# Optimization experiments

Measured on AMD Instinct MI355X. Metric: run time of the kernel, lower is better.

## Reference

```python
import jax, jax.numpy as jnp
import numpy as np

N = 50000   # nodes
E = 800000  # edges (avg degree 16)
DIMS = [(128, 128), (128, 128), (128, 64)]  # (in, out) per SAGEConv layer
EPS_BN = 1e-5
EPS_NORM = 1e-12


def _make_layer(key, din, dout):
    k1, k2 = jax.random.split(key)
    s = 1.0 / np.sqrt(din)
    return (
        jax.random.normal(k1, (dout, din), jnp.float32) * s,  # Wl: neighbor linear
        jnp.zeros((dout,), jnp.float32),                      # bl
        jax.random.normal(k2, (dout, din), jnp.float32) * s,  # Wr: root linear (no bias in PyG)
        jnp.ones((dout,), jnp.float32),                       # bn gamma
        jnp.zeros((dout,), jnp.float32),                      # bn beta
        jnp.zeros((dout,), jnp.float32),                      # bn running mean
        jnp.ones((dout,), jnp.float32),                       # bn running var
    )


def setup_inputs() -> dict:
    key = jax.random.key(0)
    kx, ke, k0, k1, k2 = jax.random.split(key, 5)
    inp = {
        "x": jax.random.normal(kx, (N, 128), jnp.float32),
        "edge_index": jax.random.randint(ke, (2, E), 0, N, dtype=jnp.int32),
    }
    for i, (k, (din, dout)) in enumerate(zip([k0, k1, k2], DIMS)):
        Wl, bl, Wr, g, b, rm, rv = _make_layer(k, din, dout)
        inp.update({f"Wl{i}": Wl, f"bl{i}": bl, f"Wr{i}": Wr,
                    f"g{i}": g, f"b{i}": b, f"rm{i}": rm, f"rv{i}": rv})
    return inp


def _sage_conv(x, src, dst, Wl, bl, Wr):
    # mean aggregation of incoming messages: gather src features, scatter-add at dst
    agg = jax.ops.segment_sum(x[src], dst, num_segments=N)          # [N, din]
    deg = jax.ops.segment_sum(jnp.ones((src.shape[0],), x.dtype), dst, num_segments=N)
    mean = agg / jnp.maximum(deg, 1.0)[:, None]
    return mean @ Wl.T + bl + x @ Wr.T


def _bn_eval(x, g, b, rm, rv):
    return g * (x - rm) * jax.lax.rsqrt(rv + EPS_BN) + b


def reference(x, edge_index,
              Wl0, bl0, Wr0, g0, b0, rm0, rv0,
              Wl1, bl1, Wr1, g1, b1, rm1, rv1,
              Wl2, bl2, Wr2, g2, b2, rm2, rv2):
    src, dst = edge_index[0], edge_index[1]
    layers = [
        (Wl0, bl0, Wr0, g0, b0, rm0, rv0),
        (Wl1, bl1, Wr1, g1, b1, rm1, rv1),
        (Wl2, bl2, Wr2, g2, b2, rm2, rv2),
    ]
    h = x
    for i, (Wl, bl, Wr, g, b, rm, rv) in enumerate(layers):
        h = _bn_eval(_sage_conv(h, src, dst, Wl, bl, Wr), g, b, rm, rv)
        if i < len(layers) - 1:
            h = jax.nn.relu(h)  # dropout is identity in eval mode
    # F.normalize(p=2, dim=1)
    return h / jnp.maximum(jnp.linalg.norm(h, axis=1, keepdims=True), EPS_NORM)
```

## Files before the change

### kernel.cpp

```cpp
#include <hip/hip_runtime.h>
#include <hip/hip_bf16.h>

#define CDIV(a,b) (((a)+(b)-1)/(b))
#define NBUCK_MAX 512

typedef __attribute__((ext_vector_type(8))) short short8;
typedef __attribute__((ext_vector_type(4))) float f32x4;
typedef __attribute__((ext_vector_type(2))) float f32x2;

static __device__ __forceinline__ unsigned short f2bf(float f){
  union { float f; unsigned u; } v; v.f = f;
  unsigned r = v.u + 0x7fffu + ((v.u >> 16) & 1u);
  return (unsigned short)(r >> 16);
}
static __device__ __forceinline__ unsigned pack2(float lo, float hi){
  return (unsigned)f2bf(lo) | ((unsigned)f2bf(hi) << 16);
}
static __device__ __forceinline__ float bf2f(unsigned short s){
  union { unsigned u; float f; } v; v.u = ((unsigned)s) << 16; return v.f;
}
static __device__ __forceinline__ unsigned pk_fp8x4(float a, float b, float c, float d){
  int v = __builtin_amdgcn_cvt_pk_fp8_f32(a, b, 0, false);
  v = __builtin_amdgcn_cvt_pk_fp8_f32(c, d, v, true);
  return (unsigned)v;
}

#define ACCQ8(v) { f32x2 p0 = __builtin_amdgcn_cvt_pk_f32_fp8((int)v.x, false); \
                   f32x2 p1 = __builtin_amdgcn_cvt_pk_f32_fp8((int)v.x, true);  \
                   f32x2 p2 = __builtin_amdgcn_cvt_pk_f32_fp8((int)v.y, false); \
                   f32x2 p3 = __builtin_amdgcn_cvt_pk_f32_fp8((int)v.y, true);  \
                   a0 += p0.x; a1 += p0.y; a2 += p1.x; a3 += p1.y; \
                   a4 += p2.x; a5 += p2.y; a6 += p3.x; a7 += p3.y; }


struct WtpArgs {
  const float *W0, *W1, *bl, *g, *b, *rm, *rv;
  unsigned short* Bpk; float *sc; float *sh;
  int kblk, dout, do_bn, nblk, perm;
};

static __device__ __forceinline__ void wtp_one(const WtpArgs& a, int idx){
  int NB16 = a.kblk*32*a.dout;
  if (idx < NB16){
    int j = idx & 7, lane = (idx >> 3) & 63, rest = idx >> 9;
    int NT = a.dout >> 4;
    int nt = rest % NT, kk = rest / NT;
    int nn = nt*16 + (lane & 15);
    int k  = kk*32 + ((lane >> 4) * 8) + j;
    float v;
    if (k < 128){
      int kc = a.perm ? (((k & 7) << 4) | (k >> 3)) : k;
      v = a.W0[nn*128 + kc];
    } else {
      v = a.W1[nn*128 + (k - 128)];
    }
    a.Bpk[idx] = f2bf(v);
  } else if (a.do_bn && idx < NB16 + a.dout){
    int jj = idx - NB16;
    float s = a.g[jj] * rsqrtf(a.rv[jj] + 1e-5f);
    a.sc[jj] = s;
    a.sh[jj] = (a.bl[jj] - a.rm[jj]) * s + a.b[jj];
  }
}


__global__ __launch_bounds__(256) void k_prep(const float* __restrict__ x, int n2, unsigned* __restrict__ xb,
                                              unsigned* __restrict__ xq,
                                              const int* __restrict__ dst, int E,
                                              int* __restrict__ bcnt, int nbuck,
                                              int castBlocks, int xqBlocks, int histBlocks,
                                              WtpArgs a0, WtpArgs a1, WtpArgs a2, WtpArgs a3){
  __shared__ int s[NBUCK_MAX];
  int b = blockIdx.x, t = threadIdx.x;
  if (b < castBlocks){
    int i = b*256 + t;
    if (i < n2){
      float2 v = ((const float2*)x)[i];
      xb[i] = pack2(v.x, v.y);
    }
    return;
  }
  b -= castBlocks;
  if (b < xqBlocks){
    int i = b*256 + t;
    if (i < (n2 >> 2)){
      int row = i >> 4, c = i & 15;
      const float* xr = x + (size_t)row*128 + c;
      float v0 = xr[0],  v1 = xr[16], v2 = xr[32],  v3 = xr[48];
      float v4 = xr[64], v5 = xr[80], v6 = xr[96],  v7 = xr[112];
      uint2 q;
      q.x = pk_fp8x4(v0, v1, v2, v3);
      q.y = pk_fp8x4(v4, v5, v6, v7);
      ((uint2*)xq)[i] = q;
    }
    return;
  }
  b -= xqBlocks;
  if (b < histBlocks){
    for (int i=t;i<nbuck;i+=256) s[i] = 0;
    __syncthreads();
    constexpr int EPT = 16;
    int e0 = b*256*EPT;
    #pragma unroll
    for (int i=0;i<EPT;i++){
      int e = e0 + i*256 + t;
      if (e < E) atomicAdd(&s[dst[e] >> 7], 1);
    }
    __syncthreads();
    for (int i=t;i<nbuck;i+=256){
      int c = s[i];
      if (c > 0) atomicAdd(&bcnt[i], c);
    }
    return;
  }
  b -= histBlocks;
  if (b < a0.nblk){ wtp_one(a0, b*256 + t); return; }
  b -= a0.nblk;
  if (b < a1.nblk){ wtp_one(a1, b*256 + t); return; }
  b -= a1.nblk;
  if (b < a2.nblk){ wtp_one(a2, b*256 + t); return; }
  b -= a2.nblk;
  wtp_one(a3, b*256 + t);
}

__global__ __launch_bounds__(256) void k_bscan(const int* __restrict__ bcnt, int nbuck,
                                               int* __restrict__ bbase){
  __shared__ int s[256];
  int t = threadIdx.x;
  int a0 = (2*t   < nbuck) ? bcnt[2*t]   : 0;
  int a1 = (2*t+1 < nbuck) ? bcnt[2*t+1] : 0;
  s[t] = a0 + a1; __syncthreads();
  for (int d=1; d<256; d<<=1){
    int u = (t>=d) ? s[t-d] : 0;
    __syncthreads();
    s[t] += u;
    __syncthreads();
  }
  int excl = s[t] - (a0 + a1);
  if (2*t   < nbuck) bbase[2*t]   = excl;
  if (2*t+1 < nbuck) bbase[2*t+1] = excl + a0;
  if (t == 255) bbase[nbuck] = s[255];
}

__global__ __launch_bounds__(256) void k_bucketA(const int* __restrict__ src, const int* __restrict__ dst,
                                                 int E, const int* __restrict__ bbase,
                                                 int* __restrict__ bcur, unsigned* __restrict__ ebuf, int nbuck){
  __shared__ int scnt[NBUCK_MAX];
  __shared__ int sbase[NBUCK_MAX];
  __shared__ int sboff[NBUCK_MAX];
  int t = threadIdx.x;
  for (int i=t;i<nbuck;i+=256) scnt[i] = 0;
  __syncthreads();
  constexpr int EPT = 16;
  int e0 = blockIdx.x*256*EPT;
  int b[EPT]; unsigned pk[EPT];
  #pragma unroll
  for (int i=0;i<EPT;i++){
    int e = e0 + i*256 + t;
    if (e < E){
      int d = dst[e];
      b[i] = d >> 7;
      pk[i] = ((unsigned)(d & 127) << 16) | (unsigned)src[e];
      atomicAdd(&scnt[b[i]], 1);
    } else b[i] = -1;
  }
  __syncthreads();
  for (int i=t;i<nbuck;i+=256){
    int c = scnt[i];
    sbase[i] = (c > 0) ? atomicAdd(&bcur[i], c) : 0;
    sboff[i] = bbase[i];
    scnt[i] = 0;
  }
  __syncthreads();
  #pragma unroll
  for (int i=0;i<EPT;i++){
    if (b[i] >= 0){
      int p = atomicAdd(&scnt[b[i]], 1);
      ebuf[(size_t)sboff[b[i]] + sbase[b[i]] + p] = pk[i];
    }
  }
}

__global__ __launch_bounds__(256) void k_bucketB(const unsigned* __restrict__ ebuf, const int* __restrict__ bbase,
                                                 int N, int* __restrict__ off, int* __restrict__ csr){
  int b = blockIdx.x;
  int n0 = b << 7, n1 = min(n0 + 128, N);
  __shared__ int sdeg[128];
  __shared__ int sabs[129];
  __shared__ int cur[128];
  int t = threadIdx.x;
  if (t < 128){ sdeg[t] = 0; cur[t] = 0; }
  __syncthreads();
  int e0 = bbase[b], e1 = bbase[b+1];
  for (int e = e0 + t; e < e1; e += 256)
    atomicAdd(&sdeg[ebuf[e] >> 16], 1);
  __syncthreads();
  for (int d=1; d<128; d<<=1){
    int u = (t < 128 && t >= d) ? sdeg[t-d] : 0;
    __syncthreads();
    if (t < 128) sdeg[t] += u;
    __syncthreads();
  }
  if (t == 0) sabs[0] = e0;
  if (t < 128) sabs[t+1] = e0 + sdeg[t];
  __syncthreads();
  if (t <= n1 - n0) off[n0 + t] = sabs[t];
  for (int e = e0 + t; e < e1; e += 256){
    unsigned pr = ebuf[e];
    int ln = (int)(pr >> 16);
    int p = atomicAdd(&cur[ln], 1);
    csr[sabs[ln] + p] = (int)(pr & 0xffffu);
  }
}


__global__ __launch_bounds__(256) void k_agg(const uint2* __restrict__ hq, const int* __restrict__ off,
                                             const int* __restrict__ csr, int n, uint4* __restrict__ mean4){
  int tid = blockIdx.x*256 + threadIdx.x;
  int lane = threadIdx.x & 63;
  int sl = lane & 15;
  int node = (tid >> 6)*4 + (lane >> 4);
  bool valid = node < n;
  int s0 = valid ? off[node]   : 0;
  int s1 = valid ? off[node+1] : 0;
  float a0=0,a1=0,a2=0,a3=0,a4=0,a5=0,a6=0,a7=0;
  int e = s0;
  for (; e + 8 <= s1; e += 8){
    int i0 = csr[e],   i1 = csr[e+1], i2 = csr[e+2], i3 = csr[e+3];
    int i4 = csr[e+4], i5 = csr[e+5], i6 = csr[e+6], i7 = csr[e+7];
    uint2 v0 = hq[(size_t)i0*16 + sl];
    uint2 v1 = hq[(size_t)i1*16 + sl];
    uint2 v2 = hq[(size_t)i2*16 + sl];
    uint2 v3 = hq[(size_t)i3*16 + sl];
    uint2 v4 = hq[(size_t)i4*16 + sl];
    uint2 v5 = hq[(size_t)i5*16 + sl];
    uint2 v6 = hq[(size_t)i6*16 + sl];
    uint2 v7 = hq[(size_t)i7*16 + sl];
    ACCQ8(v0); ACCQ8(v1); ACCQ8(v2); ACCQ8(v3);
    ACCQ8(v4); ACCQ8(v5); ACCQ8(v6); ACCQ8(v7);
  }
  for (; e + 4 <= s1; e += 4){
    int i0 = csr[e], i1 = csr[e+1], i2 = csr[e+2], i3 = csr[e+3];
    uint2 v0 = hq[(size_t)i0*16 + sl];
    uint2 v1 = hq[(size_t)i1*16 + sl];
    uint2 v2 = hq[(size_t)i2*16 + sl];
    uint2 v3 = hq[(size_t)i3*16 + sl];
    ACCQ8(v0); ACCQ8(v1); ACCQ8(v2); ACCQ8(v3);
  }
  for (; e < s1; e++){
    uint2 v = hq[(size_t)csr[e]*16 + sl];
    ACCQ8(v);
  }
  if (valid){
    int d = s1 - s0;
    float inv = 1.0f / (float)(d > 0 ? d : 1);
    uint4 o;
    o.x = pack2(a0*inv, a1*inv);
    o.y = pack2(a2*inv, a3*inv);
    o.z = pack2(a4*inv, a5*inv);
    o.w = pack2(a6*inv, a7*inv);
    mean4[(size_t)node*16 + sl] = o;
  }
}


template<bool YL>
__global__ __launch_bounds__(256, 2) void k_gemm_hid(
    const unsigned short* __restrict__ A0, const unsigned short* __restrict__ A1,
    const unsigned short* __restrict__ Bpk, const float* __restrict__ sc,
    const float* __restrict__ sh, const unsigned short* __restrict__ BpkL,
    unsigned short* __restrict__ outh, unsigned* __restrict__ outq,
    unsigned* __restrict__ outyl, int n){
  __shared__ unsigned short Bs[256*128];
  int t = threadIdx.x;
  {
    const uint4* s = (const uint4*)Bpk;
    uint4* d = (uint4*)Bs;
    #pragma unroll
    for (int i=0;i<16;i++) d[i*256 + t] = s[i*256 + t];
  }
  __syncthreads();

  int lane = t & 63, w = t >> 6;
  int quad = lane >> 4, c = lane & 15;
  int mb = blockIdx.x*128, woff = w*32;
  int r0 = mb + woff + c;
  int r1 = r0 + 16;

  f32x4 acc[2][8];
  #pragma unroll
  for (int mt=0;mt<2;mt++)
    #pragma unroll
    for (int nt=0;nt<8;nt++) acc[mt][nt] = (f32x4){0.f,0.f,0.f,0.f};

  #pragma unroll
  for (int kk=0; kk<8; kk++){
    const unsigned short* ab = (kk >= 4) ? A1 : A0;
    int ka = (kk & 3)*32 + quad*8;
    short8 a0 = {0,0,0,0,0,0,0,0}, a1 = {0,0,0,0,0,0,0,0};
    if (r0 < n) a0 = *(const short8*)(ab + (size_t)r0*128 + ka);
    if (r1 < n) a1 = *(const short8*)(ab + (size_t)r1*128 + ka);
    #pragma unroll
    for (int nt=0; nt<8; nt++){
      short8 b = *(const short8*)&Bs[(size_t)((kk*8 + nt)*64 + lane)*8];
      acc[0][nt] = __builtin_amdgcn_mfma_f32_16x16x32_bf16(a0, b, acc[0][nt], 0, 0, 0);
      acc[1][nt] = __builtin_amdgcn_mfma_f32_16x16x32_bf16(a1, b, acc[1][nt], 0, 0, 0);
    }
  }

  float scv[8], shv[8];
  #pragma unroll
  for (int nt=0;nt<8;nt++){ scv[nt] = sc[nt*16 + c]; shv[nt] = sh[nt*16 + c]; }

  #pragma unroll
  for (int mt=0; mt<2; mt++){
    #pragma unroll
    for (int r=0;r<4;r++){
      int row = mb + woff + mt*16 + quad*4 + r;
      if (row < n){
        float u[8];
        #pragma unroll
        for (int nt=0;nt<8;nt++){
          float uu = acc[mt][nt][r]*scv[nt] + shv[nt];
          u[nt] = fmaxf(uu, 0.f);
          outh[(size_t)row*128 + nt*16 + c] = f2bf(u[nt]);
        }
        if constexpr (!YL){
          uint2 q;
          q.x = pk_fp8x4(u[0], u[1], u[2], u[3]);
          q.y = pk_fp8x4(u[4], u[5], u[6], u[7]);
          ((uint2*)outq)[(size_t)row*16 + c] = q;
        }
      }
    }
  }

  if constexpr (YL){
    __syncthreads();
    {
      uint4* d = (uint4*)Bs;
      const uint4* s4 = (const uint4*)outh;
      #pragma unroll
      for (int i=0;i<8;i++){
        int idx = i*256 + t;
        int row = idx >> 4;
        int gr = mb + row; if (gr > n-1) gr = n-1;
        d[idx] = s4[(size_t)gr*16 + (idx & 15)];
      }
      const uint4* sL = (const uint4*)BpkL;
      #pragma unroll
      for (int i=0;i<4;i++) d[2048 + i*256 + t] = sL[i*256 + t];
    }
    __syncthreads();
    f32x4 acc2[2][4];
    #pragma unroll
    for (int mt=0;mt<2;mt++)
      #pragma unroll
      for (int nt=0;nt<4;nt++) acc2[mt][nt] = (f32x4){0.f,0.f,0.f,0.f};
    int r0l = woff + c, r1l = r0l + 16;
    #pragma unroll
    for (int kk=0; kk<4; kk++){
      int ka = kk*32 + quad*8;
      short8 a0 = *(const short8*)&Bs[(size_t)r0l*128 + ka];
      short8 a1 = *(const short8*)&Bs[(size_t)r1l*128 + ka];
      #pragma unroll
      for (int nt=0; nt<4; nt++){
        short8 b = *(const short8*)&Bs[16384 + (size_t)((kk*4 + nt)*64 + lane)*8];
        acc2[0][nt] = __builtin_amdgcn_mfma_f32_16x16x32_bf16(a0, b, acc2[0][nt], 0, 0, 0);
        acc2[1][nt] = __builtin_amdgcn_mfma_f32_16x16x32_bf16(a1, b, acc2[1][nt], 0, 0, 0);
      }
    }
    #pragma unroll
    for (int mt=0; mt<2; mt++){
      #pragma unroll
      for (int r=0;r<4;r++){
        int row = mb + woff + mt*16 + quad*4 + r;
        if (row < n){
          unsigned q = pk_fp8x4(acc2[0][0][r], acc2[0][1][r], acc2[0][2][r], acc2[0][3][r]);
          unsigned q1 = pk_fp8x4(acc2[1][0][r], acc2[1][1][r], acc2[1][2][r], acc2[1][3][r]);
          outyl[(size_t)row*16 + c] = (mt == 0) ? q : q1;
        }
      }
    }
  }
}


__global__ __launch_bounds__(256, 2) void k_aggf(
    const uint2* __restrict__ ylq, const int* __restrict__ off, const int* __restrict__ csr,
    const unsigned short* __restrict__ A0, const unsigned short* __restrict__ BpkR,
    const float* __restrict__ sc, const float* __restrict__ sh,
    float* __restrict__ outf, int n){
  __shared__ unsigned short Ms[128*64];
  __shared__ unsigned short Bs[128*64];
  int t = threadIdx.x;
  {
    const uint4* s = (const uint4*)BpkR;
    uint4* d = (uint4*)Bs;
    #pragma unroll
    for (int i=0;i<4;i++) d[i*256 + t] = s[i*256 + t];
  }
  int lane = t & 63, w = t >> 6;
  int mb = blockIdx.x*128;
  int sl8 = lane & 7;

  #pragma unroll
  for (int it=0; it<4; it++){
    int ln = w*32 + it*8 + (lane >> 3);
    int node = mb + ln;
    bool valid = node < n;
    int s0 = valid ? off[node]   : 0;
    int s1 = valid ? off[node+1] : 0;
    float a0=0,a1=0,a2=0,a3=0,a4=0,a5=0,a6=0,a7=0;
    int e = s0;
    for (; e + 4 <= s1; e += 4){
      int i0 = csr[e], i1 = csr[e+1], i2 = csr[e+2], i3 = csr[e+3];
      uint2 v0 = ylq[(size_t)i0*8 + sl8];
      uint2 v1 = ylq[(size_t)i1*8 + sl8];
      uint2 v2 = ylq[(size_t)i2*8 + sl8];
      uint2 v3 = ylq[(size_t)i3*8 + sl8];
      ACCQ8(v0); ACCQ8(v1); ACCQ8(v2); ACCQ8(v3);
    }
    for (; e < s1; e++){
      uint2 v = ylq[(size_t)csr[e]*8 + sl8];
      ACCQ8(v);
    }
    int d = s1 - s0;
    float inv = 1.0f / (float)(d > 0 ? d : 1);
    uint4 o;
    o.x = pack2(a0*inv, a1*inv);
    o.y = pack2(a2*inv, a3*inv);
    o.z = pack2(a4*inv, a5*inv);
    o.w = pack2(a6*inv, a7*inv);
    ((uint4*)Ms)[ln*8 + sl8] = o;
  }
  __syncthreads();

  int quad = lane >> 4, c = lane & 15;
  int woff = w*32;
  int r0 = mb + woff + c;
  int r1 = r0 + 16;
  f32x4 acc[2][4];
  #pragma unroll
  for (int mt=0;mt<2;mt++)
    #pragma unroll
    for (int nt=0;nt<4;nt++) acc[mt][nt] = (f32x4){0.f,0.f,0.f,0.f};
  #pragma unroll
  for (int kk=0; kk<4; kk++){
    int ka = kk*32 + quad*8;
    short8 a0 = {0,0,0,0,0,0,0,0}, a1 = {0,0,0,0,0,0,0,0};
    if (r0 < n) a0 = *(const short8*)(A0 + (size_t)r0*128 + ka);
    if (r1 < n) a1 = *(const short8*)(A0 + (size_t)r1*128 + ka);
    #pragma unroll
    for (int nt=0; nt<4; nt++){
      short8 b = *(const short8*)&Bs[(size_t)((kk*4 + nt)*64 + lane)*8];
      acc[0][nt] = __builtin_amdgcn_mfma_f32_16x16x32_bf16(a0, b, acc[0][nt], 0, 0, 0);
      acc[1][nt] = __builtin_amdgcn_mfma_f32_16x16x32_bf16(a1, b, acc[1][nt], 0, 0, 0);
    }
  }

  float scv[4], shv[4];
  #pragma unroll
  for (int nt=0;nt<4;nt++){ scv[nt] = sc[nt*16 + c]; shv[nt] = sh[nt*16 + c]; }

  #pragma unroll
  for (int mt=0; mt<2; mt++){
    #pragma unroll
    for (int r=0;r<4;r++){
      int lr = woff + mt*16 + quad*4 + r;
      int row = mb + lr;
      float v[4];
      float ss = 0.f;
      if (row < n){
        #pragma unroll
        for (int nt=0;nt<4;nt++){
          float u = acc[mt][nt][r] + bf2f(Ms[lr*64 + c*4 + nt]);
          u = u*scv[nt] + shv[nt];
          v[nt] = u;
          ss += u*u;
        }
      } else {
        #pragma unroll
        for (int nt=0;nt<4;nt++) v[nt] = 0.f;
      }
      ss += __shfl_xor(ss, 1, 64);
      ss += __shfl_xor(ss, 2, 64);
      ss += __shfl_xor(ss, 4, 64);
      ss += __shfl_xor(ss, 8, 64);
      float rn = 1.0f / fmaxf(sqrtf(ss), 1e-12f);
      if (row < n){
        #pragma unroll
        for (int nt=0;nt<4;nt++) outf[(size_t)row*64 + nt*16 + c] = v[nt]*rn;
      }
    }
  }
}


extern "C" void kernel_launch(void* const* d_in, const int* in_sizes, int n_in,
                              void* d_out, int out_size, void* d_ws, size_t ws_size,
                              hipStream_t stream){
  const float* x = (const float*)d_in[0];
  const int* ei  = (const int*)d_in[1];
  int N = in_sizes[0] / 128;
  int E = in_sizes[1] / 2;
  const int* esrc = ei;
  const int* edst = ei + E;
  int nbuck = CDIV(N, 128);

  const float *Wl[3], *bl[3], *Wr[3], *g[3], *bb[3], *rm[3], *rv[3];
  int dout[3];
  for (int i=0;i<3;i++){
    int base = 2 + 7*i;
    Wl[i]=(const float*)d_in[base];   bl[i]=(const float*)d_in[base+1];
    Wr[i]=(const float*)d_in[base+2]; g[i] =(const float*)d_in[base+3];
    bb[i]=(const float*)d_in[base+4]; rm[i]=(const float*)d_in[base+5];
    rv[i]=(const float*)d_in[base+6];
    dout[i] = in_sizes[base] / 128;
  }

  char* p = (char*)d_ws;
  size_t o = 0;
  auto alloc = [&](size_t bytes)->void*{ void* r = p + o; o += (bytes + 255) & ~(size_t)255; return r; };
  int* bz    = (int*)alloc((size_t)2*nbuck*4);
  int* bcnt  = bz;
  int* bcur  = bz + nbuck;
  int* bbase = (int*)alloc((size_t)(nbuck+1)*4);
  int* off   = (int*)alloc((size_t)(N+1)*4);
  int* csr   = (int*)alloc((size_t)E*4);
  unsigned* ebuf = (unsigned*)alloc((size_t)E*4);
  unsigned* xb   = (unsigned*)alloc((size_t)N*64*4);
  unsigned* xq   = (unsigned*)alloc((size_t)N*128);
  unsigned* mb   = (unsigned*)alloc((size_t)N*64*4);
  unsigned* h_a  = (unsigned*)alloc((size_t)N*64*4);
  unsigned* haq  = (unsigned*)alloc((size_t)N*128);
  unsigned* h_b  = (unsigned*)alloc((size_t)N*64*4);
  unsigned* ylb  = (unsigned*)alloc((size_t)N*64);
  unsigned short* Bpk01[2];
  float* sc[3]; float* sh[3];
  for (int i=0;i<2;i++) Bpk01[i] = (unsigned short*)alloc((size_t)256*dout[i]*2);
  unsigned short* BpkL = (unsigned short*)alloc((size_t)128*dout[2]*2);
  unsigned short* BpkR = (unsigned short*)alloc((size_t)128*dout[2]*2);
  for (int i=0;i<3;i++){
    sc[i] = (float*)alloc((size_t)dout[i]*4);
    sh[i] = (float*)alloc((size_t)dout[i]*4);
  }

  hipMemsetAsync(bz, 0, (size_t)2*nbuck*4, stream);

  WtpArgs wa[4];
  wa[0] = { Wl[0], Wr[0], bl[0], g[0], bb[0], rm[0], rv[0], Bpk01[0], sc[0], sh[0], 8, dout[0], 1, CDIV(256*dout[0]+dout[0],256), 1 };
  wa[1] = { Wl[1], Wr[1], bl[1], g[1], bb[1], rm[1], rv[1], Bpk01[1], sc[1], sh[1], 8, dout[1], 1, CDIV(256*dout[1]+dout[1],256), 1 };
  wa[2] = { Wl[2], nullptr, nullptr, nullptr, nullptr, nullptr, nullptr, BpkL, nullptr, nullptr, 4, dout[2], 0, CDIV(128*dout[2],256), 0 };
  wa[3] = { Wr[2], nullptr, bl[2], g[2], bb[2], rm[2], rv[2], BpkR, sc[2], sh[2], 4, dout[2], 1, CDIV(128*dout[2]+dout[2],256), 0 };

  int castBlocks = CDIV(N*64, 256);
  int xqBlocks   = CDIV(N*16, 256);
  int histBlocks = CDIV(E, 256*16);
  int prepBlocks = castBlocks + xqBlocks + histBlocks + wa[0].nblk + wa[1].nblk + wa[2].nblk + wa[3].nblk;
  k_prep   <<<prepBlocks,256,0,stream>>>(x, N*64, xb, xq, edst, E, bcnt, nbuck, castBlocks, xqBlocks, histBlocks,
                                         wa[0], wa[1], wa[2], wa[3]);
  k_bscan  <<<1,256,0,stream>>>(bcnt, nbuck, bbase);
  k_bucketA<<<CDIV(E,256*16),256,0,stream>>>(esrc, edst, E, bbase, bcur, ebuf, nbuck);
  k_bucketB<<<nbuck,256,0,stream>>>(ebuf, bbase, N, off, csr);

  k_agg<<<CDIV(N*16,256),256,0,stream>>>((const uint2*)xq, off, csr, N, (uint4*)mb);
  k_gemm_hid<false><<<CDIV(N,128),256,0,stream>>>((const unsigned short*)mb, (const unsigned short*)xb,
                                                  Bpk01[0], sc[0], sh[0], nullptr,
                                                  (unsigned short*)h_a, haq, nullptr, N);
  k_agg<<<CDIV(N*16,256),256,0,stream>>>((const uint2*)haq, off, csr, N, (uint4*)mb);
  k_gemm_hid<true><<<CDIV(N,128),256,0,stream>>>((const unsigned short*)mb, (const unsigned short*)h_a,
                                                 Bpk01[1], sc[1], sh[1], BpkL,
                                                 (unsigned short*)h_b, nullptr, ylb, N);
  k_aggf<<<CDIV(N,128),256,0,stream>>>((const uint2*)ylb, off, csr,
                                       (const unsigned short*)h_b, BpkR, sc[2], sh[2],
                                       (float*)d_out, N);
}
```

Before: 250.0 us.

## Widen aggregation gathers to 16-byte loads and stage CSR indices in LDS

The aggregation kernels now have each lane gather 16 fp8 features with a uint4 load instead of 8 with a uint2, so fewer lanes serve each node (8 per node in k_agg, 4 in k_aggf). Each block first copies its contiguous CSR index range into shared memory, falling back to global reads past a fixed cap. The x fp8 quantization is folded into the bf16 cast pass with a natural column order, and the layer-0 weight permutation is dropped to match. This targets gather transaction count and repeated index loads, at the cost of more registers per thread and fewer threads working on each node.

```diff
diff --git a/kernel.cpp b/kernel.cpp
--- a/kernel.cpp
+++ b/kernel.cpp
@@ -3,6 +3,8 @@
 
 #define CDIV(a,b) (((a)+(b)-1)/(b))
 #define NBUCK_MAX 512
+#define AGG_CAP  1536
+#define AGGF_CAP 3072
 
 typedef __attribute__((ext_vector_type(8))) short short8;
 typedef __attribute__((ext_vector_type(4))) float f32x4;
@@ -25,12 +27,18 @@
   return (unsigned)v;
 }
 
-#define ACCQ8(v) { f32x2 p0 = __builtin_amdgcn_cvt_pk_f32_fp8((int)v.x, false); \
-                   f32x2 p1 = __builtin_amdgcn_cvt_pk_f32_fp8((int)v.x, true);  \
-                   f32x2 p2 = __builtin_amdgcn_cvt_pk_f32_fp8((int)v.y, false); \
-                   f32x2 p3 = __builtin_amdgcn_cvt_pk_f32_fp8((int)v.y, true);  \
-                   a0 += p0.x; a1 += p0.y; a2 += p1.x; a3 += p1.y; \
-                   a4 += p2.x; a5 += p2.y; a6 += p3.x; a7 += p3.y; }
+#define ACCQ16(v) { f32x2 q0 = __builtin_amdgcn_cvt_pk_f32_fp8((int)v.x, false); \
+                    f32x2 q1 = __builtin_amdgcn_cvt_pk_f32_fp8((int)v.x, true);  \
+                    f32x2 q2 = __builtin_amdgcn_cvt_pk_f32_fp8((int)v.y, false); \
+                    f32x2 q3 = __builtin_amdgcn_cvt_pk_f32_fp8((int)v.y, true);  \
+                    f32x2 q4 = __builtin_amdgcn_cvt_pk_f32_fp8((int)v.z, false); \
+                    f32x2 q5 = __builtin_amdgcn_cvt_pk_f32_fp8((int)v.z, true);  \
+                    f32x2 q6 = __builtin_amdgcn_cvt_pk_f32_fp8((int)v.w, false); \
+                    f32x2 q7 = __builtin_amdgcn_cvt_pk_f32_fp8((int)v.w, true);  \
+                    a0 += q0.x; a1 += q0.y; a2  += q1.x; a3  += q1.y; \
+                    a4 += q2.x; a5 += q2.y; a6  += q3.x; a7  += q3.y; \
+                    a8 += q4.x; a9 += q4.y; a10 += q5.x; a11 += q5.y; \
+                    a12 += q6.x; a13 += q6.y; a14 += q7.x; a15 += q7.y; }
 
 
 struct WtpArgs {
@@ -64,38 +72,25 @@
 }
 
 
-__global__ __launch_bounds__(256) void k_prep(const float* __restrict__ x, int n2, unsigned* __restrict__ xb,
+__global__ __launch_bounds__(256) void k_prep(const float* __restrict__ x, int n4, unsigned* __restrict__ xb,
                                               unsigned* __restrict__ xq,
                                               const int* __restrict__ dst, int E,
                                               int* __restrict__ bcnt, int nbuck,
-                                              int castBlocks, int xqBlocks, int histBlocks,
+                                              int castBlocks, int histBlocks,
                                               WtpArgs a0, WtpArgs a1, WtpArgs a2, WtpArgs a3){
   __shared__ int s[NBUCK_MAX];
   int b = blockIdx.x, t = threadIdx.x;
   if (b < castBlocks){
     int i = b*256 + t;
-    if (i < n2){
-      float2 v = ((const float2*)x)[i];
-      xb[i] = pack2(v.x, v.y);
+    if (i < n4){
+      float4 v = ((const float4*)x)[i];
+      uint2 o; o.x = pack2(v.x, v.y); o.y = pack2(v.z, v.w);
+      ((uint2*)xb)[i] = o;
+      xq[i] = pk_fp8x4(v.x, v.y, v.z, v.w);
     }
     return;
   }
   b -= castBlocks;
-  if (b < xqBlocks){
-    int i = b*256 + t;
-    if (i < (n2 >> 2)){
-      int row = i >> 4, c = i & 15;
-      const float* xr = x + (size_t)row*128 + c;
-      float v0 = xr[0],  v1 = xr[16], v2 = xr[32],  v3 = xr[48];
-      float v4 = xr[64], v5 = xr[80], v6 = xr[96],  v7 = xr[112];
-      uint2 q;
-      q.x = pk_fp8x4(v0, v1, v2, v3);
-      q.y = pk_fp8x4(v4, v5, v6, v7);
-      ((uint2*)xq)[i] = q;
-    }
-    return;
-  }
-  b -= xqBlocks;
   if (b < histBlocks){
     for (int i=t;i<nbuck;i+=256) s[i] = 0;
     __syncthreads();
@@ -214,52 +209,80 @@
 }
 
 
-__global__ __launch_bounds__(256) void k_agg(const uint2* __restrict__ hq, const int* __restrict__ off,
+__global__ __launch_bounds__(256) void k_agg(const uint4* __restrict__ hq4, const int* __restrict__ off,
                                              const int* __restrict__ csr, int n, uint4* __restrict__ mean4){
-  int tid = blockIdx.x*256 + threadIdx.x;
-  int lane = threadIdx.x & 63;
-  int sl = lane & 15;
-  int node = (tid >> 6)*4 + (lane >> 4);
+  __shared__ int scsr[AGG_CAP];
+  __shared__ int sw[2];
+  int t = threadIdx.x;
+  int nodeblk = blockIdx.x * 32;
+  if (t < 2) sw[t] = off[min(nodeblk + t*32, n)];
+  __syncthreads();
+  int e0b = sw[0];
+  int span = sw[1] - e0b;
+  for (int i = t; i < span && i < AGG_CAP; i += 256) scsr[i] = csr[e0b + i];
+  __syncthreads();
+
+  int lane = t & 63;
+  int sl = lane & 7;
+  int node = nodeblk + (t >> 3);
   bool valid = node < n;
   int s0 = valid ? off[node]   : 0;
   int s1 = valid ? off[node+1] : 0;
   float a0=0,a1=0,a2=0,a3=0,a4=0,a5=0,a6=0,a7=0;
+  float a8=0,a9=0,a10=0,a11=0,a12=0,a13=0,a14=0,a15=0;
   int e = s0;
   for (; e + 8 <= s1; e += 8){
-    int i0 = csr[e],   i1 = csr[e+1], i2 = csr[e+2], i3 = csr[e+3];
-    int i4 = csr[e+4], i5 = csr[e+5], i6 = csr[e+6], i7 = csr[e+7];
-    uint2 v0 = hq[(size_t)i0*16 + sl];
-    uint2 v1 = hq[(size_t)i1*16 + sl];
-    uint2 v2 = hq[(size_t)i2*16 + sl];
-    uint2 v3 = hq[(size_t)i3*16 + sl];
-    uint2 v4 = hq[(size_t)i4*16 + sl];
-    uint2 v5 = hq[(size_t)i5*16 + sl];
-    uint2 v6 = hq[(size_t)i6*16 + sl];
-    uint2 v7 = hq[(size_t)i7*16 + sl];
-    ACCQ8(v0); ACCQ8(v1); ACCQ8(v2); ACCQ8(v3);
-    ACCQ8(v4); ACCQ8(v5); ACCQ8(v6); ACCQ8(v7);
+    int le = e - e0b;
+    int i0,i1,i2,i3,i4,i5,i6,i7;
+    if (le + 8 <= AGG_CAP){
+      i0 = scsr[le];   i1 = scsr[le+1]; i2 = scsr[le+2]; i3 = scsr[le+3];
+      i4 = scsr[le+4]; i5 = scsr[le+5]; i6 = scsr[le+6]; i7 = scsr[le+7];
+    } else {
+      i0 = csr[e];   i1 = csr[e+1]; i2 = csr[e+2]; i3 = csr[e+3];
+      i4 = csr[e+4]; i5 = csr[e+5]; i6 = csr[e+6]; i7 = csr[e+7];
+    }
+    uint4 v0 = hq4[(size_t)i0*8 + sl];
+    uint4 v1 = hq4[(size_t)i1*8 + sl];
+    uint4 v2 = hq4[(size_t)i2*8 + sl];
+    uint4 v3 = hq4[(size_t)i3*8 + sl];
+    uint4 v4 = hq4[(size_t)i4*8 + sl];
+    uint4 v5 = hq4[(size_t)i5*8 + sl];
+    uint4 v6 = hq4[(size_t)i6*8 + sl];
+    uint4 v7 = hq4[(size_t)i7*8 + sl];
+    ACCQ16(v0); ACCQ16(v1); ACCQ16(v2); ACCQ16(v3);
+    ACCQ16(v4); ACCQ16(v5); ACCQ16(v6); ACCQ16(v7);
   }
   for (; e + 4 <= s1; e += 4){
-    int i0 = csr[e], i1 = csr[e+1], i2 = csr[e+2], i3 = csr[e+3];
-    uint2 v0 = hq[(size_t)i0*16 + sl];
-    uint2 v1 = hq[(size_t)i1*16 + sl];
-    uint2 v2 = hq[(size_t)i2*16 + sl];
-    uint2 v3 = hq[(size_t)i3*16 + sl];
-    ACCQ8(v0); ACCQ8(v1); ACCQ8(v2); ACCQ8(v3);
+    int le = e - e0b;
+    int i0,i1,i2,i3;
+    if (le + 4 <= AGG_CAP){
+      i0 = scsr[le]; i1 = scsr[le+1]; i2 = scsr[le+2]; i3 = scsr[le+3];
+    } else {
+      i0 = csr[e]; i1 = csr[e+1]; i2 = csr[e+2]; i3 = csr[e+3];
+    }
+    uint4 v0 = hq4[(size_t)i0*8 + sl];
+    uint4 v1 = hq4[(size_t)i1*8 + sl];
+    uint4 v2 = hq4[(size_t)i2*8 + sl];
+    uint4 v3 = hq4[(size_t)i3*8 + sl];
+    ACCQ16(v0); ACCQ16(v1); ACCQ16(v2); ACCQ16(v3);
   }
   for (; e < s1; e++){
-    uint2 v = hq[(size_t)csr[e]*16 + sl];
-    ACCQ8(v);
+    int le = e - e0b;
+    int ii = (le < AGG_CAP) ? scsr[le] : csr[e];
+    uint4 v = hq4[(size_t)ii*8 + sl];
+    ACCQ16(v);
   }
   if (valid){
     int d = s1 - s0;
     float inv = 1.0f / (float)(d > 0 ? d : 1);
-    uint4 o;
-    o.x = pack2(a0*inv, a1*inv);
-    o.y = pack2(a2*inv, a3*inv);
-    o.z = pack2(a4*inv, a5*inv);
-    o.w = pack2(a6*inv, a7*inv);
-    mean4[(size_t)node*16 + sl] = o;
+    uint4 o0, o1;
+    o0.x = pack2(a0*inv,  a1*inv);  o0.y = pack2(a2*inv,  a3*inv);
+    o0.z = pack2(a4*inv,  a5*inv);  o0.w = pack2(a6*inv,  a7*inv);
+    o1.x = pack2(a8*inv,  a9*inv);  o1.y = pack2(a10*inv, a11*inv);
+    o1.z = pack2(a12*inv, a13*inv); o1.w = pack2(a14*inv, a15*inv);
+    size_t base = (size_t)node*16 + (size_t)sl*2;
+    mean4[base]   = o0;
+    mean4[base+1] = o1;
   }
 }
 
@@ -387,52 +410,92 @@
 
 
 __global__ __launch_bounds__(256, 2) void k_aggf(
-    const uint2* __restrict__ ylq, const int* __restrict__ off, const int* __restrict__ csr,
+    const uint4* __restrict__ ylq4, const int* __restrict__ off, const int* __restrict__ csr,
     const unsigned short* __restrict__ A0, const unsigned short* __restrict__ BpkR,
     const float* __restrict__ sc, const float* __restrict__ sh,
     float* __restrict__ outf, int n){
   __shared__ unsigned short Ms[128*64];
   __shared__ unsigned short Bs[128*64];
+  __shared__ int scsr[AGGF_CAP];
+  __shared__ int sw[2];
   int t = threadIdx.x;
+  int mb = blockIdx.x*128;
+  if (t < 2) sw[t] = off[min(mb + t*128, n)];
   {
     const uint4* s = (const uint4*)BpkR;
     uint4* d = (uint4*)Bs;
     #pragma unroll
     for (int i=0;i<4;i++) d[i*256 + t] = s[i*256 + t];
   }
+  __syncthreads();
+  int e0b = sw[0];
+  int span = sw[1] - e0b;
+  for (int i = t; i < span && i < AGGF_CAP; i += 256) scsr[i] = csr[e0b + i];
+  __syncthreads();
+
   int lane = t & 63, w = t >> 6;
-  int mb = blockIdx.x*128;
-  int sl8 = lane & 7;
-
-  #pragma unroll
-  for (int it=0; it<4; it++){
-    int ln = w*32 + it*8 + (lane >> 3);
+  int sl4 = lane & 3;
+
+  #pragma unroll
+  for (int it=0; it<2; it++){
+    int ln = w*32 + it*16 + (lane >> 2);
     int node = mb + ln;
     bool valid = node < n;
     int s0 = valid ? off[node]   : 0;
     int s1 = valid ? off[node+1] : 0;
     float a0=0,a1=0,a2=0,a3=0,a4=0,a5=0,a6=0,a7=0;
+    float a8=0,a9=0,a10=0,a11=0,a12=0,a13=0,a14=0,a15=0;
     int e = s0;
+    for (; e + 8 <= s1; e += 8){
+      int le = e - e0b;
+      int i0,i1,i2,i3,i4,i5,i6,i7;
+      if (le + 8 <= AGGF_CAP){
+        i0 = scsr[le];   i1 = scsr[le+1]; i2 = scsr[le+2]; i3 = scsr[le+3];
+        i4 = scsr[le+4]; i5 = scsr[le+5]; i6 = scsr[le+6]; i7 = scsr[le+7];
+      } else {
+        i0 = csr[e];   i1 = csr[e+1]; i2 = csr[e+2]; i3 = csr[e+3];
+        i4 = csr[e+4]; i5 = csr[e+5]; i6 = csr[e+6]; i7 = csr[e+7];
+      }
+      uint4 v0 = ylq4[(size_t)i0*4 + sl4];
+      uint4 v1 = ylq4[(size_t)i1*4 + sl4];
+      uint4 v2 = ylq4[(size_t)i2*4 + sl4];
+      uint4 v3 = ylq4[(size_t)i3*4 + sl4];
+      uint4 v4 = ylq4[(size_t)i4*4 + sl4];
+      uint4 v5 = ylq4[(size_t)i5*4 + sl4];
+      uint4 v6 = ylq4[(size_t)i6*4 + sl4];
+      uint4 v7 = ylq4[(size_t)i7*4 + sl4];
+      ACCQ16(v0); ACCQ16(v1); ACCQ16(v2); ACCQ16(v3);
+      ACCQ16(v4); ACCQ16(v5); ACCQ16(v6); ACCQ16(v7);
+    }
     for (; e + 4 <= s1; e += 4){
-      int i0 = csr[e], i1 = csr[e+1], i2 = csr[e+2], i3 = csr[e+3];
-      uint2 v0 = ylq[(size_t)i0*8 + sl8];
-      uint2 v1 = ylq[(size_t)i1*8 + sl8];
-      uint2 v2 = ylq[(size_t)i2*8 + sl8];
-      uint2 v3 = ylq[(size_t)i3*8 + sl8];
-      ACCQ8(v0); ACCQ8(v1); ACCQ8(v2); ACCQ8(v3);
+      int le = e - e0b;
+      int i0,i1,i2,i3;
+      if (le + 4 <= AGGF_CAP){
+        i0 = scsr[le]; i1 = scsr[le+1]; i2 = scsr[le+2]; i3 = scsr[le+3];
+      } else {
+        i0 = csr[e]; i1 = csr[e+1]; i2 = csr[e+2]; i3 = csr[e+3];
+      }
+      uint4 v0 = ylq4[(size_t)i0*4 + sl4];
+      uint4 v1 = ylq4[(size_t)i1*4 + sl4];
+      uint4 v2 = ylq4[(size_t)i2*4 + sl4];
+      uint4 v3 = ylq4[(size_t)i3*4 + sl4];
+      ACCQ16(v0); ACCQ16(v1); ACCQ16(v2); ACCQ16(v3);
     }
     for (; e < s1; e++){
-      uint2 v = ylq[(size_t)csr[e]*8 + sl8];
-      ACCQ8(v);
+      int le = e - e0b;
+      int ii = (le < AGGF_CAP) ? scsr[le] : csr[e];
+      uint4 v = ylq4[(size_t)ii*4 + sl4];
+      ACCQ16(v);
     }
     int d = s1 - s0;
     float inv = 1.0f / (float)(d > 0 ? d : 1);
-    uint4 o;
-    o.x = pack2(a0*inv, a1*inv);
-    o.y = pack2(a2*inv, a3*inv);
-    o.z = pack2(a4*inv, a5*inv);
-    o.w = pack2(a6*inv, a7*inv);
-    ((uint4*)Ms)[ln*8 + sl8] = o;
+    uint4 o0, o1;
+    o0.x = pack2(a0*inv,  a1*inv);  o0.y = pack2(a2*inv,  a3*inv);
+    o0.z = pack2(a4*inv,  a5*inv);  o0.w = pack2(a6*inv,  a7*inv);
+    o1.x = pack2(a8*inv,  a9*inv);  o1.y = pack2(a10*inv, a11*inv);
+    o1.z = pack2(a12*inv, a13*inv); o1.w = pack2(a14*inv, a15*inv);
+    ((uint4*)Ms)[ln*8 + sl4*2]     = o0;
+    ((uint4*)Ms)[ln*8 + sl4*2 + 1] = o1;
   }
   __syncthreads();
 
@@ -549,30 +612,29 @@
   hipMemsetAsync(bz, 0, (size_t)2*nbuck*4, stream);
 
   WtpArgs wa[4];
-  wa[0] = { Wl[0], Wr[0], bl[0], g[0], bb[0], rm[0], rv[0], Bpk01[0], sc[0], sh[0], 8, dout[0], 1, CDIV(256*dout[0]+dout[0],256), 1 };
+  wa[0] = { Wl[0], Wr[0], bl[0], g[0], bb[0], rm[0], rv[0], Bpk01[0], sc[0], sh[0], 8, dout[0], 1, CDIV(256*dout[0]+dout[0],256), 0 };
   wa[1] = { Wl[1], Wr[1], bl[1], g[1], bb[1], rm[1], rv[1], Bpk01[1], sc[1], sh[1], 8, dout[1], 1, CDIV(256*dout[1]+dout[1],256), 1 };
   wa[2] = { Wl[2], nullptr, nullptr, nullptr, nullptr, nullptr, nullptr, BpkL, nullptr, nullptr, 4, dout[2], 0, CDIV(128*dout[2],256), 0 };
   wa[3] = { Wr[2], nullptr, bl[2], g[2], bb[2], rm[2], rv[2], BpkR, sc[2], sh[2], 4, dout[2], 1, CDIV(128*dout[2]+dout[2],256), 0 };
 
-  int castBlocks = CDIV(N*64, 256);
-  int xqBlocks   = CDIV(N*16, 256);
+  int castBlocks = CDIV(N*32, 256);
   int histBlocks = CDIV(E, 256*16);
-  int prepBlocks = castBlocks + xqBlocks + histBlocks + wa[0].nblk + wa[1].nblk + wa[2].nblk + wa[3].nblk;
-  k_prep   <<<prepBlocks,256,0,stream>>>(x, N*64, xb, xq, edst, E, bcnt, nbuck, castBlocks, xqBlocks, histBlocks,
+  int prepBlocks = castBlocks + histBlocks + wa[0].nblk + wa[1].nblk + wa[2].nblk + wa[3].nblk;
+  k_prep   <<<prepBlocks,256,0,stream>>>(x, N*32, xb, xq, edst, E, bcnt, nbuck, castBlocks, histBlocks,
                                          wa[0], wa[1], wa[2], wa[3]);
   k_bscan  <<<1,256,0,stream>>>(bcnt, nbuck, bbase);
   k_bucketA<<<CDIV(E,256*16),256,0,stream>>>(esrc, edst, E, bbase, bcur, ebuf, nbuck);
   k_bucketB<<<nbuck,256,0,stream>>>(ebuf, bbase, N, off, csr);
 
-  k_agg<<<CDIV(N*16,256),256,0,stream>>>((const uint2*)xq, off, csr, N, (uint4*)mb);
+  k_agg<<<CDIV(N,32),256,0,stream>>>((const uint4*)xq, off, csr, N, (uint4*)mb);
   k_gemm_hid<false><<<CDIV(N,128),256,0,stream>>>((const unsigned short*)mb, (const unsigned short*)xb,
                                                   Bpk01[0], sc[0], sh[0], nullptr,
                                                   (unsigned short*)h_a, haq, nullptr, N);
-  k_agg<<<CDIV(N*16,256),256,0,stream>>>((const uint2*)haq, off, csr, N, (uint4*)mb);
+  k_agg<<<CDIV(N,32),256,0,stream>>>((const uint4*)haq, off, csr, N, (uint4*)mb);
   k_gemm_hid<true><<<CDIV(N,128),256,0,stream>>>((const unsigned short*)mb, (const unsigned short*)h_a,
                                                  Bpk01[1], sc[1], sh[1], BpkL,
                                                  (unsigned short*)h_b, nullptr, ylb, N);
-  k_aggf<<<CDIV(N,128),256,0,stream>>>((const uint2*)ylb, off, csr,
+  k_aggf<<<CDIV(N,128),256,0,stream>>>((const uint4*)ylb, off, csr,
                                        (const unsigned short*)h_b, BpkR, sc[2], sh[2],
                                        (float*)d_out, N);
 }
```

Result: faster. 240.2 us (-3.9%).
